# Optimization experiments

Measured on AMD Instinct MI355X. Metric: run time of the kernel, lower is better.

The kernel has to match this reference:

```python
import jax, jax.numpy as jnp
import numpy as np

T, B = 100, 128
EMB, RDIM, SDIM = 64, 32, 32
IN = EMB + RDIM + SDIM  # 128 = rnn_input_dim
H = 512                 # rnn_output_dim
ITEMS = 10000


def setup_inputs() -> dict:
    key = jax.random.key(0)
    ks = jax.random.split(key, 12)
    k_lstm = 1.0 / np.sqrt(H).astype(np.float32)
    k_lin = 1.0 / np.sqrt(H + SDIM).astype(np.float32)
    return {
        "pre_actions": jax.random.randint(ks[0], (T, B), 0, ITEMS),
        "pre_rewards": jax.random.uniform(ks[1], (T, B), jnp.float32),
        "pre_statistic": jax.random.normal(ks[2], (T, B, SDIM), jnp.float32),
        "hx": jnp.zeros((B, H), jnp.float32),
        "cx": jnp.zeros((B, H), jnp.float32),
        "emb_table": jax.random.normal(ks[3], (ITEMS, EMB), jnp.float32) * 0.02,
        "W_ih": jax.random.uniform(ks[4], (4 * H, IN), jnp.float32, -k_lstm, k_lstm),
        "W_hh": jax.random.uniform(ks[5], (4 * H, H), jnp.float32, -k_lstm, k_lstm),
        "b_ih": jax.random.uniform(ks[6], (4 * H,), jnp.float32, -k_lstm, k_lstm),
        "b_hh": jax.random.uniform(ks[7], (4 * H,), jnp.float32, -k_lstm, k_lstm),
        "W_lin": jax.random.uniform(ks[8], (ITEMS, H + SDIM), jnp.float32, -k_lin, k_lin),
        "b_lin": jax.random.uniform(ks[9], (ITEMS,), jnp.float32, -k_lin, k_lin),
    }


def reference(pre_actions, pre_rewards, pre_statistic, hx, cx,
              emb_table, W_ih, W_hh, b_ih, b_hh, W_lin, b_lin):
    # Embedding lookup + one-hot reward bucket + statistic concat: [T,B,IN]
    emb = emb_table[pre_actions]                                   # [T,B,EMB]
    idx = jnp.floor(RDIM * (2.0 - pre_rewards) / 4.0).astype(jnp.int32)
    one_hot = jax.nn.one_hot(idx, RDIM, dtype=emb.dtype)           # [T,B,RDIM]
    ars = jnp.concatenate([emb, one_hot, pre_statistic], axis=-1)  # [T,B,IN]

    # Precompute input projections for all timesteps (batched GEMM)
    x_proj = jnp.einsum('tbi,gi->tbg', ars, W_ih) + b_ih + b_hh    # [T,B,4H]

    def step(carry, xp):
        h, c = carry
        gates = xp + h @ W_hh.T                                    # [B,4H]
        i, f, g, o = jnp.split(gates, 4, axis=-1)                  # torch LSTMCell gate order i,f,g,o
        i = jax.nn.sigmoid(i)
        f = jax.nn.sigmoid(f)
        g = jnp.tanh(g)
        o = jax.nn.sigmoid(o)
        c = f * c + i * g
        h = o * jnp.tanh(c)
        return (h, c), h

    _, hs = jax.lax.scan(step, (hx, cx), x_proj)                   # hs: [T,B,H]

    lin_in = jnp.concatenate([hs, pre_statistic], axis=-1)         # [T,B,H+SDIM]
    pn_outputs = jnp.einsum('tbd,vd->tbv', lin_in, W_lin) + b_lin  # [T,B,ITEMS]

    l2_norm = jnp.linalg.norm(W_lin) + jnp.linalg.norm(b_lin)      # sum of Frobenius norms of linear params
    return pn_outputs, l2_norm
```

## Files before the change

kernel.cpp:

```cpp
#include <hip/hip_runtime.h>
#include <math.h>
#include <stdint.h>

#define T_STEPS 100
#define BATCH   128
#define EMB     64
#define RDIM    32
#define SDIM    32
#define INDIM   128
#define HDIM    512
#define G4      2048
#define ITEMS   10000
#define NPAD    10112
#define TBROWS  12800
#define KLIN    544

typedef unsigned short u16;
typedef __attribute__((ext_vector_type(8))) short  bf16x8;
typedef __attribute__((ext_vector_type(4))) float  f32x4;

__device__ __forceinline__ u16 f2bf(float x) {
  unsigned u = __float_as_uint(x);
  u = u + 0x7fffu + ((u >> 16) & 1u);
  return (u16)(u >> 16);
}
__device__ __forceinline__ float bf2f(u16 b) { return __uint_as_float(((unsigned)b) << 16); }

#define OFF_SYNC   0UL
#define OFF_XPROJ  512UL
#define OFF_LININ  52429312UL
#define OFF_WLIN   66355712UL
#define OFF_WHH    77357568UL
#define OFF_WIH    79454720UL
#define OFF_ARS    79979008UL
#define OFF_BIAS   83255808UL
#define OFF_HBUF   83264000UL

#define HBUFE 65536
#define GSLAB 16384
#define WPG   8

__global__ void prep_kernel(const int* __restrict__ pa, const float* __restrict__ pr,
                            const float* __restrict__ ps, const float* __restrict__ hx,
                            const float* __restrict__ emb,
                            const float* __restrict__ W_ih, const float* __restrict__ W_hh,
                            const float* __restrict__ b_ih, const float* __restrict__ b_hh,
                            const float* __restrict__ W_lin, const float* __restrict__ b_lin,
                            u16* __restrict__ ars, u16* __restrict__ lin_in,
                            u16* __restrict__ wlin, u16* __restrict__ whh, u16* __restrict__ wih,
                            float* __restrict__ bias2, u16* __restrict__ hbuf,
                            float* __restrict__ acc) {
  const int tid0 = blockIdx.x * blockDim.x + threadIdx.x;
  const int np = gridDim.x * blockDim.x;
  float sw = 0.f, sb = 0.f;
  for (int i = tid0; i < NPAD * KLIN; i += np) {
    int v = i / KLIN;
    float x = (v < ITEMS) ? W_lin[i] : 0.f;
    wlin[i] = f2bf(x);
    sw += x * x;
  }
  for (int i = tid0; i < ITEMS; i += np) { float x = b_lin[i]; sb += x * x; }
  for (int i = tid0; i < G4 * HDIM; i += np) {
    int gp = i >> 9, k = i & 511;
    int g = (gp & 3) * 512 + (gp >> 2);
    whh[i] = f2bf(W_hh[g * HDIM + k]);
  }
  for (int i = tid0; i < G4 * INDIM; i += np) {
    int gp = i >> 7, k = i & 127;
    int g = (gp & 3) * 512 + (gp >> 2);
    wih[i] = f2bf(W_ih[g * INDIM + k]);
  }
  for (int i = tid0; i < G4; i += np) {
    int g = (i & 3) * 512 + (i >> 2);
    bias2[i] = b_ih[g] + b_hh[g];
  }
  for (int i = tid0; i < TBROWS * INDIM; i += np) {
    int tb = i >> 7, k = i & 127;
    float v;
    if (k < EMB) {
      v = emb[pa[tb] * EMB + k];
    } else if (k < EMB + RDIM) {
      int idx = (int)floorf((float)RDIM * (2.0f - pr[tb]) * 0.25f);
      v = ((k - EMB) == idx) ? 1.0f : 0.0f;
    } else {
      v = ps[tb * SDIM + (k - EMB - RDIM)];
    }
    ars[i] = f2bf(v);
  }
  for (int i = tid0; i < TBROWS * SDIM; i += np) {
    int tb = i >> 5, s = i & 31;
    lin_in[(size_t)tb * KLIN + HDIM + s] = f2bf(ps[i]);
  }
  for (int i = tid0; i < BATCH * HDIM; i += np) {
    int b = i >> 9, k = i & 511;
    hbuf[(((size_t)(b >> 5) * 64 + (k >> 3)) * 32 + (b & 31)) * 8 + (k & 7)] = f2bf(hx[i]);
  }
  __shared__ float red[2][8];
  for (int off = 32; off > 0; off >>= 1) { sw += __shfl_down(sw, off); sb += __shfl_down(sb, off); }
  int lane = threadIdx.x & 63, wv = threadIdx.x >> 6;
  if (lane == 0) { red[0][wv] = sw; red[1][wv] = sb; }
  __syncthreads();
  if (threadIdx.x == 0) {
    float a = 0.f, b = 0.f;
    for (int w = 0; w < (int)(blockDim.x >> 6); ++w) { a += red[0][w]; b += red[1][w]; }
    atomicAdd(&acc[0], a);
    atomicAdd(&acc[1], b);
  }
}

__global__ void l2_kernel(const float* __restrict__ acc, float* __restrict__ out) {
  out[0] = sqrtf(acc[0]) + sqrtf(acc[1]);
}

template <int EPI>
__global__ __launch_bounds__(256) void gemm_bt(const u16* __restrict__ A, const u16* __restrict__ Bm,
                                               const float* __restrict__ bias, void* __restrict__ Cout,
                                               int K, int N) {
  __shared__ u16 Asm[128 * 32];
  __shared__ u16 Bsm[128 * 32];
  const int tid = threadIdx.x;
  const int lane = tid & 63;
  const int wv = tid >> 6;
  const int wm = wv >> 1, wn = wv & 1;
  const int l15 = lane & 15, quad = lane >> 4;
  const int mt = blockIdx.y, nt = blockIdx.x;
  const u16* Ag = A + (size_t)mt * 128 * K;
  const u16* Bg = Bm + (size_t)nt * 128 * K;
  f32x4 acc[4][4] = {};

  for (int k0 = 0; k0 < K; k0 += 32) {
    __syncthreads();
    {
      int e = tid * 8;
      int row = e >> 5, col = e & 31;
      *(bf16x8*)&Asm[e]        = *(const bf16x8*)&Ag[(size_t)row * K + k0 + col];
      *(bf16x8*)&Asm[e + 2048] = *(const bf16x8*)&Ag[(size_t)(row + 64) * K + k0 + col];
      *(bf16x8*)&Bsm[e]        = *(const bf16x8*)&Bg[(size_t)row * K + k0 + col];
      *(bf16x8*)&Bsm[e + 2048] = *(const bf16x8*)&Bg[(size_t)(row + 64) * K + k0 + col];
    }
    __syncthreads();
    bf16x8 af[4], bfr[4];
#pragma unroll
    for (int mi = 0; mi < 4; ++mi)
      af[mi] = *(const bf16x8*)&Asm[(wm * 64 + mi * 16 + l15) * 32 + quad * 8];
#pragma unroll
    for (int ni = 0; ni < 4; ++ni)
      bfr[ni] = *(const bf16x8*)&Bsm[(wn * 64 + ni * 16 + l15) * 32 + quad * 8];
#pragma unroll
    for (int mi = 0; mi < 4; ++mi)
#pragma unroll
      for (int ni = 0; ni < 4; ++ni)
        acc[mi][ni] = __builtin_amdgcn_mfma_f32_16x16x32_bf16(af[mi], bfr[ni], acc[mi][ni], 0, 0, 0);
  }
#pragma unroll
  for (int mi = 0; mi < 4; ++mi) {
#pragma unroll
    for (int ni = 0; ni < 4; ++ni) {
      int ng = nt * 128 + wn * 64 + ni * 16 + l15;
      float bv = (EPI == 0 || ng < N) ? bias[ng] : 0.0f;
#pragma unroll
      for (int r = 0; r < 4; ++r) {
        int mg = mt * 128 + wm * 64 + mi * 16 + quad * 4 + r;
        float v = acc[mi][ni][r] + bv;
        if (EPI == 0) {
          ((u16*)Cout)[(size_t)mg * N + ng] = f2bf(v);
        } else {
          if (ng < N) ((float*)Cout)[(size_t)mg * (size_t)N + ng] = v;
        }
      }
    }
  }
}

__global__ __launch_bounds__(512, 2) void lstm_kernel(const u16* __restrict__ xproj,
                                                      const u16* __restrict__ whh,
                                                      const float* __restrict__ cx,
                                                      u16* __restrict__ hbuf,
                                                      u16* __restrict__ lin_in,
                                                      unsigned* __restrict__ cnt) {
  __shared__ u16 hls[GSLAB];
  const int tid = threadIdx.x;
  const int lane = tid & 63, wv = tid >> 6;
  const int grp = blockIdx.x >> 3;
  const int wg8 = blockIdx.x & 7;
  const int cb = wg8 * 8 + wv;
  const int l15 = lane & 15, quad = lane >> 4;
  const int b0 = grp * 32;
  unsigned* mycnt = cnt + grp * 16;

  bf16x8 wa[2][16];
  {
    const u16* wp = whh + (size_t)(cb * 32) * HDIM;
#pragma unroll
    for (int sm = 0; sm < 2; ++sm)
#pragma unroll
      for (int kk = 0; kk < 16; ++kk)
        wa[sm][kk] = *(const bf16x8*)&wp[(size_t)(sm * 16 + l15) * HDIM + kk * 32 + quad * 8];
  }
  float c[2][2];
#pragma unroll
  for (int sm = 0; sm < 2; ++sm)
#pragma unroll
    for (int sn = 0; sn < 2; ++sn)
      c[sm][sn] = cx[(size_t)(b0 + sn * 16 + l15) * HDIM + cb * 8 + sm * 4 + quad];

  const u16* xpb = xproj + (size_t)b0 * G4 + cb * 32;
  uint2 xpv[2][2];
#pragma unroll
  for (int sm = 0; sm < 2; ++sm)
#pragma unroll
    for (int sn = 0; sn < 2; ++sn)
      xpv[sm][sn] = *(const uint2*)&xpb[(size_t)(sn * 16 + l15) * G4 + sm * 16 + quad * 4];

  for (int t = 0; t < T_STEPS; ++t) {
    const u16* hsrc = hbuf + (size_t)(t & 1) * HBUFE + (size_t)grp * GSLAB;
#pragma unroll
    for (int s = tid; s < GSLAB / 8; s += 512)
      *(bf16x8*)&hls[s * 8] = *(const bf16x8*)&hsrc[s * 8];
    __syncthreads();

    f32x4 acc[2][2] = {};
#pragma unroll
    for (int kk = 0; kk < 16; ++kk) {
      bf16x8 h0v = *(const bf16x8*)&hls[(((kk * 4 + quad) * 32) + l15) * 8];
      bf16x8 h1v = *(const bf16x8*)&hls[(((kk * 4 + quad) * 32) + 16 + l15) * 8];
      acc[0][0] = __builtin_amdgcn_mfma_f32_16x16x32_bf16(wa[0][kk], h0v, acc[0][0], 0, 0, 0);
      acc[0][1] = __builtin_amdgcn_mfma_f32_16x16x32_bf16(wa[0][kk], h1v, acc[0][1], 0, 0, 0);
      acc[1][0] = __builtin_amdgcn_mfma_f32_16x16x32_bf16(wa[1][kk], h0v, acc[1][0], 0, 0, 0);
      acc[1][1] = __builtin_amdgcn_mfma_f32_16x16x32_bf16(wa[1][kk], h1v, acc[1][1], 0, 0, 0);
    }

    const size_t trow = (size_t)t * BATCH + b0;
    u16* hdst = hbuf + (size_t)((t + 1) & 1) * HBUFE + (size_t)grp * GSLAB;
#pragma unroll
    for (int sm = 0; sm < 2; ++sm)
#pragma unroll
      for (int sn = 0; sn < 2; ++sn) {
        uint2 pk = xpv[sm][sn];
        float gi = acc[sm][sn][0] + bf2f((u16)(pk.x & 0xffffu));
        float gf = acc[sm][sn][1] + bf2f((u16)(pk.x >> 16));
        float gg = acc[sm][sn][2] + bf2f((u16)(pk.y & 0xffffu));
        float go = acc[sm][sn][3] + bf2f((u16)(pk.y >> 16));
        gi = 1.f / (1.f + __expf(-gi));
        gf = 1.f / (1.f + __expf(-gf));
        gg = 1.f - 2.f / (__expf(2.f * gg) + 1.f);
        go = 1.f / (1.f + __expf(-go));
        float cn = gf * c[sm][sn] + gi * gg;
        c[sm][sn] = cn;
        float hv = go * (1.f - 2.f / (__expf(2.f * cn) + 1.f));
        u16 hb = f2bf(hv);
        int b = sn * 16 + l15;
        int jlow = sm * 4 + quad;
        hdst[(size_t)((cb * 32 + b) * 8) + jlow] = hb;
        lin_in[(trow + b) * KLIN + cb * 8 + jlow] = hb;
      }

    if (t + 1 < T_STEPS) {
#pragma unroll
      for (int sm = 0; sm < 2; ++sm)
#pragma unroll
        for (int sn = 0; sn < 2; ++sn)
          xpv[sm][sn] = *(const uint2*)&xpb[(size_t)((t + 1) * BATCH + sn * 16 + l15) * G4 +
                                            sm * 16 + quad * 4];
    }

    __syncthreads();
    if (tid == 0) {
      __threadfence();
      atomicAdd(mycnt, 1u);
      const unsigned target = (unsigned)(WPG * (t + 1));
      while (__hip_atomic_load(mycnt, __ATOMIC_RELAXED, __HIP_MEMORY_SCOPE_AGENT) < target)
        __builtin_amdgcn_s_sleep(1);
      __threadfence();
    }
    __syncthreads();
  }
}

extern "C" void kernel_launch(void* const* d_in, const int* in_sizes, int n_in,
                              void* d_out, int out_size, void* d_ws, size_t ws_size,
                              hipStream_t stream) {
  const int*   pa   = (const int*)d_in[0];
  const float* pr   = (const float*)d_in[1];
  const float* ps   = (const float*)d_in[2];
  const float* hx   = (const float*)d_in[3];
  const float* cxp  = (const float*)d_in[4];
  const float* emb  = (const float*)d_in[5];
  const float* wih  = (const float*)d_in[6];
  const float* whh  = (const float*)d_in[7];
  const float* bih  = (const float*)d_in[8];
  const float* bhh  = (const float*)d_in[9];
  const float* wlin = (const float*)d_in[10];
  const float* blin = (const float*)d_in[11];

  char* ws = (char*)d_ws;
  unsigned* cnt   = (unsigned*)(ws + OFF_SYNC);
  float*    acc   = (float*)(ws + 256);
  u16* xprojW = (u16*)(ws + OFF_XPROJ);
  u16* lininW = (u16*)(ws + OFF_LININ);
  u16* wlinW  = (u16*)(ws + OFF_WLIN);
  u16* whhW   = (u16*)(ws + OFF_WHH);
  u16* wihW   = (u16*)(ws + OFF_WIH);
  u16* arsW   = (u16*)(ws + OFF_ARS);
  float* biasW = (float*)(ws + OFF_BIAS);
  u16* hbufW  = (u16*)(ws + OFF_HBUF);
  float* outF = (float*)d_out;

  hipMemsetAsync(d_ws, 0, 512, stream);

  prep_kernel<<<dim3(2048), dim3(256), 0, stream>>>(
      pa, pr, ps, hx, emb, wih, whh, bih, bhh, wlin, blin,
      arsW, lininW, wlinW, whhW, wihW, biasW, hbufW, acc);

  l2_kernel<<<dim3(1), dim3(1), 0, stream>>>(acc, outF + (size_t)out_size - 1);

  gemm_bt<0><<<dim3(16, 100), dim3(256), 0, stream>>>(arsW, wihW, biasW, (void*)xprojW, INDIM, G4);

  lstm_kernel<<<dim3(32), dim3(512), 0, stream>>>(xprojW, whhW, cxp, hbufW, lininW, cnt);

  gemm_bt<1><<<dim3(79, 100), dim3(256), 0, stream>>>(lininW, wlinW, blin, (void*)outF, KLIN, ITEMS);
}
```

Before: 1.598 ms.

## Restage LSTM hidden-state exchange through swizzled LDS with relaxed atomics and no fences

Changes the global h buffer to a row-major per-group layout and stages the new h values through a small swizzled LDS tile, so each thread writes one 8-byte chunk to global instead of scattered 2-byte stores. The LDS copy of h is XOR-swizzled to avoid bank conflicts. Blocks are remapped so groups interleave across block IDs. The grid barrier drops its __threadfence calls and relies on relaxed agent-scope atomic loads and stores for visibility. Removing the fences risks memory-ordering races between the h stores and the counter increment.

```diff
diff --git a/kernel.cpp b/kernel.cpp
--- a/kernel.cpp
+++ b/kernel.cpp
@@ -16,6 +16,7 @@
 #define KLIN    544
 
 typedef unsigned short u16;
+typedef unsigned long long u64;
 typedef __attribute__((ext_vector_type(8))) short  bf16x8;
 typedef __attribute__((ext_vector_type(4))) float  f32x4;
 
@@ -93,7 +94,7 @@
   }
   for (int i = tid0; i < BATCH * HDIM; i += np) {
     int b = i >> 9, k = i & 511;
-    hbuf[(((size_t)(b >> 5) * 64 + (k >> 3)) * 32 + (b & 31)) * 8 + (k & 7)] = f2bf(hx[i]);
+    hbuf[(size_t)(b >> 5) * GSLAB + (size_t)(b & 31) * HDIM + k] = f2bf(hx[i]);
   }
   __shared__ float red[2][8];
   for (int off = 32; off > 0; off >>= 1) { sw += __shfl_down(sw, off); sb += __shfl_down(sb, off); }
@@ -179,10 +180,11 @@
                                                       u16* __restrict__ lin_in,
                                                       unsigned* __restrict__ cnt) {
   __shared__ u16 hls[GSLAB];
+  __shared__ u16 hout[32 * 64];
   const int tid = threadIdx.x;
   const int lane = tid & 63, wv = tid >> 6;
-  const int grp = blockIdx.x >> 3;
-  const int wg8 = blockIdx.x & 7;
+  const int grp = blockIdx.x & 3;
+  const int wg8 = blockIdx.x >> 2;
   const int cb = wg8 * 8 + wv;
   const int l15 = lane & 15, quad = lane >> 4;
   const int b0 = grp * 32;
@@ -194,8 +196,10 @@
 #pragma unroll
     for (int sm = 0; sm < 2; ++sm)
 #pragma unroll
-      for (int kk = 0; kk < 16; ++kk)
+      for (int kk = 0; kk < 16; ++kk) {
         wa[sm][kk] = *(const bf16x8*)&wp[(size_t)(sm * 16 + l15) * HDIM + kk * 32 + quad * 8];
+        asm volatile("" : "+v"(wa[sm][kk]));
+      }
   }
   float c[2][2];
 #pragma unroll
@@ -212,26 +216,37 @@
     for (int sn = 0; sn < 2; ++sn)
       xpv[sm][sn] = *(const uint2*)&xpb[(size_t)(sn * 16 + l15) * G4 + sm * 16 + quad * 4];
 
+  char* hlsb = (char*)hls;
+  char* houtb = (char*)hout;
+
   for (int t = 0; t < T_STEPS; ++t) {
-    const u16* hsrc = hbuf + (size_t)(t & 1) * HBUFE + (size_t)grp * GSLAB;
-#pragma unroll
-    for (int s = tid; s < GSLAB / 8; s += 512)
-      *(bf16x8*)&hls[s * 8] = *(const bf16x8*)&hsrc[s * 8];
+    {
+      const u64* hs = (const u64*)(hbuf + (size_t)(t & 1) * HBUFE + (size_t)grp * GSLAB);
+      u64 tmp[8];
+#pragma unroll
+      for (int i = 0; i < 8; ++i)
+        tmp[i] = __hip_atomic_load(hs + tid + i * 512, __ATOMIC_RELAXED, __HIP_MEMORY_SCOPE_AGENT);
+#pragma unroll
+      for (int i = 0; i < 8; ++i) {
+        int o = (tid + i * 512) * 8;
+        int b = o >> 10, col = o & 1023;
+        *(u64*)&hlsb[b * 1024 + (col ^ ((b & 7) << 4))] = tmp[i];
+      }
+    }
     __syncthreads();
 
     f32x4 acc[2][2] = {};
 #pragma unroll
     for (int kk = 0; kk < 16; ++kk) {
-      bf16x8 h0v = *(const bf16x8*)&hls[(((kk * 4 + quad) * 32) + l15) * 8];
-      bf16x8 h1v = *(const bf16x8*)&hls[(((kk * 4 + quad) * 32) + 16 + l15) * 8];
+      int csw = (kk * 64 + quad * 16) ^ ((l15 & 7) << 4);
+      bf16x8 h0v = *(const bf16x8*)&hlsb[l15 * 1024 + csw];
+      bf16x8 h1v = *(const bf16x8*)&hlsb[(16 + l15) * 1024 + csw];
       acc[0][0] = __builtin_amdgcn_mfma_f32_16x16x32_bf16(wa[0][kk], h0v, acc[0][0], 0, 0, 0);
       acc[0][1] = __builtin_amdgcn_mfma_f32_16x16x32_bf16(wa[0][kk], h1v, acc[0][1], 0, 0, 0);
       acc[1][0] = __builtin_amdgcn_mfma_f32_16x16x32_bf16(wa[1][kk], h0v, acc[1][0], 0, 0, 0);
       acc[1][1] = __builtin_amdgcn_mfma_f32_16x16x32_bf16(wa[1][kk], h1v, acc[1][1], 0, 0, 0);
     }
 
-    const size_t trow = (size_t)t * BATCH + b0;
-    u16* hdst = hbuf + (size_t)((t + 1) & 1) * HBUFE + (size_t)grp * GSLAB;
 #pragma unroll
     for (int sm = 0; sm < 2; ++sm)
 #pragma unroll
@@ -248,12 +263,20 @@
         float cn = gf * c[sm][sn] + gi * gg;
         c[sm][sn] = cn;
         float hv = go * (1.f - 2.f / (__expf(2.f * cn) + 1.f));
-        u16 hb = f2bf(hv);
         int b = sn * 16 + l15;
-        int jlow = sm * 4 + quad;
-        hdst[(size_t)((cb * 32 + b) * 8) + jlow] = hb;
-        lin_in[(trow + b) * KLIN + cb * 8 + jlow] = hb;
+        int colb = (wv * 8 + sm * 4 + quad) * 2;
+        *(u16*)&houtb[b * 128 + (colb ^ ((b & 7) << 3))] = f2bf(hv);
       }
+    __syncthreads();
+
+    {
+      int b = tid >> 4, c8 = (tid & 15) * 8;
+      u64 hv = *(const u64*)&houtb[b * 128 + (c8 ^ ((b & 7) << 3))];
+      u16* gdst = hbuf + (size_t)((t + 1) & 1) * HBUFE + (size_t)grp * GSLAB +
+                  (size_t)b * HDIM + wg8 * 64 + (tid & 15) * 4;
+      __hip_atomic_store((u64*)gdst, hv, __ATOMIC_RELAXED, __HIP_MEMORY_SCOPE_AGENT);
+      *(u64*)&lin_in[((size_t)t * BATCH + b0 + b) * KLIN + wg8 * 64 + (tid & 15) * 4] = hv;
+    }
 
     if (t + 1 < T_STEPS) {
 #pragma unroll
@@ -266,12 +289,10 @@
 
     __syncthreads();
     if (tid == 0) {
-      __threadfence();
-      atomicAdd(mycnt, 1u);
+      __hip_atomic_fetch_add(mycnt, 1u, __ATOMIC_RELAXED, __HIP_MEMORY_SCOPE_AGENT);
       const unsigned target = (unsigned)(WPG * (t + 1));
       while (__hip_atomic_load(mycnt, __ATOMIC_RELAXED, __HIP_MEMORY_SCOPE_AGENT) < target)
         __builtin_amdgcn_s_sleep(1);
-      __threadfence();
     }
     __syncthreads();
   }
```

Result: faster. 1.296 ms (-18.9%).
